# Kernel tuning notes

Measured on AMD Instinct MI355X. Metric: run time of the kernel, lower is better.

The kernel has to match this reference:

```python
import jax, jax.numpy as jnp
import numpy as np

N, K, A, LOCAL, PAIR = 1024, 48, 5, 512, 128
RBF_BINS = 16

def _normalize(v, eps=1e-8):
    return v / jnp.sqrt(jnp.sum(v * v, axis=-1, keepdims=True) + eps)

def _frames(pos):
    # pos: (N, A, 3); backbone frame from N(0), CA(1), C(2) via Gram-Schmidt
    n, ca, c = pos[:, 0], pos[:, 1], pos[:, 2]
    e1 = _normalize(c - ca)
    v2 = n - ca
    e2 = _normalize(v2 - jnp.sum(v2 * e1, -1, keepdims=True) * e1)
    e3 = jnp.cross(e1, e2)
    R = jnp.stack([e1, e2, e3], axis=-1)  # (N,3,3) columns are frame axes
    return R, ca

def _rbf(d, d_min=0.0, d_max=22.0, bins=RBF_BINS):
    centers = jnp.linspace(d_min, d_max, bins)
    step = (d_max - d_min) / bins
    return jnp.exp(-((d[..., None] - centers) / step) ** 2)

def setup_inputs():
    key = jax.random.key(0)
    ks = jax.random.split(key, 16)
    def rn(k, shape, scale=1.0):
        return (scale * jax.random.normal(k, shape)).astype(jnp.float32)
    local = rn(ks[0], (N, LOCAL))
    pos = rn(ks[1], (N, A, 3), 3.0)
    pair = rn(ks[2], (N, N, PAIR), 0.1)
    neighbours = jax.random.randint(ks[3], (N, K), 0, N).astype(jnp.int32)
    mask = jnp.ones((N,), dtype=bool)
    d_dist = A * A * RBF_BINS   # 400
    d_dir = A * A * 3           # 75
    d_vec = 2 * A * 3           # 30
    s = lambda f: 1.0 / np.sqrt(f)
    return dict(
        local=local, pos=pos, pair=pair, neighbours=neighbours, mask=mask,
        W_li=rn(ks[4], (LOCAL, PAIR), s(LOCAL)),
        W_lj=rn(ks[5], (LOCAL, PAIR), s(LOCAL)),
        W_dist=rn(ks[6], (d_dist, PAIR), s(d_dist)),
        W_dir=rn(ks[7], (d_dir, PAIR), s(d_dir)),
        W_rot=rn(ks[8], (9, PAIR), s(9)),
        W_vec=rn(ks[9], (d_vec, PAIR), s(d_vec)),
        ln_scale=jnp.ones((PAIR,), jnp.float32),
        ln_bias=jnp.zeros((PAIR,), jnp.float32),
        mlp_w1=rn(ks[10], (PAIR, 2 * PAIR), s(PAIR)),
        mlp_b1=jnp.zeros((2 * PAIR,), jnp.float32),
        mlp_w2=rn(ks[11], (2 * PAIR, PAIR), s(2 * PAIR)),
        mlp_b2=jnp.zeros((PAIR,), jnp.float32),
    )

def reference(local, pos, pair, neighbours, mask,
              W_li, W_lj, W_dist, W_dir, W_rot, W_vec,
              ln_scale, ln_bias, mlp_w1, mlp_b1, mlp_w2, mlp_b2):
    n_idx = jnp.arange(neighbours.shape[0])
    pair_mask = (mask[:, None] & mask[neighbours]) & (neighbours != -1)
    p = pair[n_idx[:, None], neighbours]                      # (N,K,PAIR) gather
    R, t = _frames(pos)                                       # (N,3,3), (N,3)
    pos_nb = pos[neighbours]                                  # (N,K,A,3)
    # source / target node feature projections
    p = p + (local @ W_li)[:, None] + (local @ W_lj)[neighbours]
    # distance features: all atom-pair distances, RBF-encoded in [0, 22]
    off = pos[:, None, :, None, :] - pos_nb[:, :, None, :, :] # (N,K,A,A,3)
    dist = jnp.sqrt(jnp.sum(off * off, -1) + 1e-8)            # (N,K,A,A)
    p = p + _rbf(dist).reshape(*neighbours.shape, -1) @ W_dist
    # direction features: atom-pair offsets in the local frame, normalized
    off_local = jnp.einsum('nij,nkabi->nkabj', R, off)
    p = p + _normalize(off_local).reshape(*neighbours.shape, -1) @ W_dir
    # relative rotation features: R_i^T R_j, flattened
    R_rel = jnp.einsum('nai,nkaj->nkij', R, R[neighbours])
    p = p + R_rel.reshape(*neighbours.shape, 9) @ W_rot
    # pair vector features: self and neighbour atoms in the local frame (x0.1)
    x_self = jnp.einsum('nij,nai->naj', R, pos - t[:, None])            # (N,A,3)
    x_nb = jnp.einsum('nij,nkai->nkaj', R, pos_nb - t[:, None, None])   # (N,K,A,3)
    vec = jnp.concatenate(
        (0.1 * jnp.broadcast_to(x_self[:, None], x_nb.shape), 0.1 * x_nb),
        axis=-1).reshape(*neighbours.shape, -1)
    p = p + vec @ W_vec
    # LayerNorm (scale + offset)
    mu = jnp.mean(p, -1, keepdims=True)
    var = jnp.var(p, -1, keepdims=True)
    p = (p - mu) * jax.lax.rsqrt(var + 1e-5) * ln_scale + ln_bias
    # MLP: hidden 2*PAIR, gelu, linear out
    p = jax.nn.gelu(p @ mlp_w1 + mlp_b1) @ mlp_w2 + mlp_b2
    return p, pair_mask
```

## Files before the change

### kernel.cpp

```cpp
#include <hip/hip_runtime.h>
#include <hip/hip_bf16.h>
#include <math.h>

#define N 1024
#define K 48
#define A 5
#define LOCALD 512
#define PAIRD 128
#define ROWS 32
#define FEATK 544
#define SF_STRIDE_B 1152

#define WS_R  0
#define WS_T  (WS_R + N*9)
#define WS_XS (WS_T + N*3)
#define WS_LI (WS_XS + N*15)
#define WS_LJ (WS_LI + N*128)
#define WCT_OFF 1159168u
#define W1T_OFF 1298432u
#define W2T_OFF 1363968u

typedef _Float16 half8 __attribute__((ext_vector_type(8)));
typedef float f32x16 __attribute__((ext_vector_type(16)));

__device__ __forceinline__ float gelu_fast(float x) {
    float u2 = 1.5957691216057308f * x * (1.0f + 0.044715f * x * x);
    float t = __expf(-u2);
    return x * __builtin_amdgcn_rcpf(1.0f + t);
}

__global__ __launch_bounds__(256) void prep_kernel(
    const float* __restrict__ local_, const float* __restrict__ pos,
    const float* __restrict__ W_li, const float* __restrict__ W_lj,
    const float* __restrict__ Wd, const float* __restrict__ Wdir,
    const float* __restrict__ Wrot, const float* __restrict__ Wv,
    const float* __restrict__ w1, const float* __restrict__ w2,
    float* __restrict__ ws, char* __restrict__ wsb)
{
    const int tid = threadIdx.x;
    if (blockIdx.x >= 256) {
        _Float16* wct = (_Float16*)(wsb + WCT_OFF);
        _Float16* w1t = (_Float16*)(wsb + W1T_OFF);
        _Float16* w2t = (_Float16*)(wsb + W2T_OFF);
        int g = (blockIdx.x - 256) * 256 + tid;
        if (g < 128 * 544) {
            int c = g & 127, f = g >> 7;
            float v = 0.0f;
            if (f < 400) v = Wd[(size_t)f * 128 + c];
            else if (f < 475) v = Wdir[(size_t)(f - 400) * 128 + c];
            else if (f < 484) v = Wrot[(size_t)(f - 475) * 128 + c];
            else if (f < 514) v = Wv[(size_t)(f - 484) * 128 + c];
            wct[(size_t)c * FEATK + f] = (_Float16)v;
        } else {
            int g2 = g - 128 * 544;
            if (g2 < 256 * 128) {
                int c = g2 & 255, f = g2 >> 8;
                w1t[(size_t)c * 128 + f] = (_Float16)w1[(size_t)f * 256 + c];
            } else {
                int g3 = g2 - 256 * 128;
                if (g3 < 128 * 256) {
                    int c = g3 & 127, f = g3 >> 7;
                    w2t[(size_t)c * 256 + f] = (_Float16)w2[(size_t)f * 128 + c];
                }
            }
        }
        return;
    }

    const int n0 = blockIdx.x * 4;
    __shared__ float sl[4][LOCALD];
    __shared__ float sR4[4][9];
    __shared__ float st4[4][3];

    for (int t = tid; t < 4 * LOCALD; t += 256) {
        int r = t >> 9, q = t & 511;
        sl[r][q] = local_[(size_t)(n0 + r) * LOCALD + q];
    }
    if (tid < 4) {
        int n = n0 + tid;
        const float* pp = pos + (size_t)n * 15;
        float nx = pp[0], ny = pp[1], nz = pp[2];
        float cax = pp[3], cay = pp[4], caz = pp[5];
        float cx = pp[6], cy = pp[7], cz = pp[8];
        float e1x = cx - cax, e1y = cy - cay, e1z = cz - caz;
        float inv1 = rsqrtf(e1x * e1x + e1y * e1y + e1z * e1z + 1e-8f);
        e1x *= inv1; e1y *= inv1; e1z *= inv1;
        float v2x = nx - cax, v2y = ny - cay, v2z = nz - caz;
        float dp = v2x * e1x + v2y * e1y + v2z * e1z;
        float e2x = v2x - dp * e1x, e2y = v2y - dp * e1y, e2z = v2z - dp * e1z;
        float inv2 = rsqrtf(e2x * e2x + e2y * e2y + e2z * e2z + 1e-8f);
        e2x *= inv2; e2y *= inv2; e2z *= inv2;
        float e3x = e1y * e2z - e1z * e2y;
        float e3y = e1z * e2x - e1x * e2z;
        float e3z = e1x * e2y - e1y * e2x;
        sR4[tid][0] = e1x; sR4[tid][1] = e2x; sR4[tid][2] = e3x;
        sR4[tid][3] = e1y; sR4[tid][4] = e2y; sR4[tid][5] = e3y;
        sR4[tid][6] = e1z; sR4[tid][7] = e2z; sR4[tid][8] = e3z;
        st4[tid][0] = cax; st4[tid][1] = cay; st4[tid][2] = caz;
        #pragma unroll
        for (int i = 0; i < 9; ++i) ws[WS_R + (size_t)n * 9 + i] = sR4[tid][i];
        #pragma unroll
        for (int i = 0; i < 3; ++i) ws[WS_T + (size_t)n * 3 + i] = st4[tid][i];
    }
    __syncthreads();

    for (int t = tid; t < 4 * 15; t += 256) {
        int r = t / 15, q = t % 15, a = q / 3, dd = q % 3;
        int n = n0 + r;
        const float* pp = pos + (size_t)n * 15 + a * 3;
        float v = sR4[r][0 * 3 + dd] * (pp[0] - st4[r][0])
                + sR4[r][1 * 3 + dd] * (pp[1] - st4[r][1])
                + sR4[r][2 * 3 + dd] * (pp[2] - st4[r][2]);
        ws[WS_XS + (size_t)n * 15 + q] = v;
    }

    const int c = tid & 127;
    const int hh = tid >> 7;
    const int r0 = hh * 2;
    float ali0 = 0, ali1 = 0, alj0 = 0, alj1 = 0;
    const float* wli = W_li + c;
    const float* wlj = W_lj + c;
    #pragma unroll 8
    for (int f = 0; f < LOCALD; ++f) {
        float a_ = wli[(size_t)f * 128];
        float b_ = wlj[(size_t)f * 128];
        float l0 = sl[r0 + 0][f], l1 = sl[r0 + 1][f];
        ali0 += l0 * a_; ali1 += l1 * a_;
        alj0 += l0 * b_; alj1 += l1 * b_;
    }
    ws[WS_LI + (size_t)(n0 + r0 + 0) * 128 + c] = ali0;
    ws[WS_LI + (size_t)(n0 + r0 + 1) * 128 + c] = ali1;
    ws[WS_LJ + (size_t)(n0 + r0 + 0) * 128 + c] = alj0;
    ws[WS_LJ + (size_t)(n0 + r0 + 1) * 128 + c] = alj1;
}

__device__ __forceinline__ void sfw(char* smem, int r, int f, float v) {
    int off = r * SF_STRIDE_B + ((f * 2) ^ ((r & 7) << 4));
    *(_Float16*)(smem + off) = (_Float16)v;
}

__global__ __launch_bounds__(256, 3) void main_kernel(
    const float* __restrict__ pair, const float* __restrict__ pos,
    const int* __restrict__ neigh, const int* __restrict__ mask,
    const float* __restrict__ ln_s, const float* __restrict__ ln_b,
    const float* __restrict__ b1, const float* __restrict__ b2,
    const float* __restrict__ ws, const char* __restrict__ wsb,
    float* __restrict__ out)
{
    const int R0 = blockIdx.x * ROWS;
    const int tid = threadIdx.x;
    const int lane = tid & 63;
    const int wv = tid >> 6;
    const int myrow = lane & 31;
    const int khalf = (lane >> 5) * 8;
    const int hi = lane >> 5;
    const int swz = (myrow & 7) << 4;

    __shared__ __align__(16) char smem[45184];
    int*   sn  = (int*)(smem + 36864);
    int*   sj  = (int*)(smem + 36992);
    float* spn = (float*)(smem + 37120);
    float* spj = (float*)(smem + 39040);
    float* srn = (float*)(smem + 40960);
    float* srj = (float*)(smem + 42112);
    float* sxs = (float*)(smem + 43264);

    const _Float16* wct = (const _Float16*)(wsb + WCT_OFF);
    const int colbase = wv * 32 + myrow;

    if (tid < ROWS) {
        int Rg = R0 + tid;
        int n = Rg / K;
        int kk = Rg - n * K;
        int j = neigh[n * K + kk];
        if (j < 0) j += N;
        sn[tid] = n; sj[tid] = j;
    }
    __syncthreads();

    const int n0 = R0 / K;
    const int n1 = (n0 + 1 < N) ? n0 + 1 : n0;
    float li0 = ws[WS_LI + (size_t)n0 * PAIRD + colbase];
    float li1 = ws[WS_LI + (size_t)n1 * PAIRD + colbase];
    float pv[16];
    #pragma unroll
    for (int q = 0; q < 16; ++q) {
        int rr = (q & 3) + 8 * (q >> 2) + 4 * hi;
        int nq = sn[rr], jq = sj[rr];
        float li = (nq == n0) ? li0 : li1;
        pv[q] = pair[((size_t)nq * N + jq) * PAIRD + colbase]
              + ws[WS_LJ + (size_t)jq * PAIRD + colbase] + li;
    }

    for (int t = tid; t < ROWS * 15; t += 256) {
        int r = t / 15, q = t % 15;
        spn[t] = pos[(size_t)sn[r] * 15 + q];
        spj[t] = pos[(size_t)sj[r] * 15 + q];
        sxs[t] = ws[WS_XS + (size_t)sn[r] * 15 + q];
    }
    for (int t = tid; t < ROWS * 9; t += 256) {
        int r = t / 9, q = t % 9;
        srn[t] = ws[WS_R + (size_t)sn[r] * 9 + q];
        srj[t] = ws[WS_R + (size_t)sj[r] * 9 + q];
    }
    __syncthreads();

    for (int t = tid; t < ROWS * 30; t += 256) {
        int r = t / 30, f = 514 + t % 30;
        sfw(smem, r, f, 0.0f);
    }

    for (int t = tid; t < ROWS * 25; t += 256) {
        int r = t / 25, ab = t % 25, a = ab / 5, b = ab % 5;
        const float* Pn = spn + r * 15;
        const float* Pj = spj + r * 15;
        const float* Rn = srn + r * 9;
        float o0 = Pn[a * 3 + 0] - Pj[b * 3 + 0];
        float o1 = Pn[a * 3 + 1] - Pj[b * 3 + 1];
        float o2 = Pn[a * 3 + 2] - Pj[b * 3 + 2];
        float d = sqrtf(o0 * o0 + o1 * o1 + o2 * o2 + 1e-8f);
        float z = d * (16.0f / 22.0f);
        int base = a * 80 + b * 16;
        int rb = r * SF_STRIDE_B;
        int rsw = (r & 7) << 4;
        #pragma unroll
        for (int bp = 0; bp < 8; ++bp) {
            float e0 = __expf(-z * z);
            float z1 = z - 1.0666666666666667f;
            float e1 = __expf(-z1 * z1);
            z = z1 - 1.0666666666666667f;
            union { _Float16 h[2]; unsigned u; } pk;
            pk.h[0] = (_Float16)e0; pk.h[1] = (_Float16)e1;
            int off = rb + (((base + bp * 2) * 2) ^ rsw);
            *(unsigned*)(smem + off) = pk.u;
        }
        float l0 = Rn[0] * o0 + Rn[3] * o1 + Rn[6] * o2;
        float l1 = Rn[1] * o0 + Rn[4] * o1 + Rn[7] * o2;
        float l2 = Rn[2] * o0 + Rn[5] * o1 + Rn[8] * o2;
        float inv = rsqrtf(l0 * l0 + l1 * l1 + l2 * l2 + 1e-8f);
        int dbase = 400 + a * 15 + b * 3;
        sfw(smem, r, dbase + 0, l0 * inv);
        sfw(smem, r, dbase + 1, l1 * inv);
        sfw(smem, r, dbase + 2, l2 * inv);
    }
    for (int t = tid; t < ROWS * 9; t += 256) {
        int r = t / 9, q = t % 9, i = q / 3, jd = q % 3;
        const float* Rn = srn + r * 9;
        const float* Rj = srj + r * 9;
        float v = Rn[0 * 3 + i] * Rj[0 * 3 + jd]
                + Rn[1 * 3 + i] * Rj[1 * 3 + jd]
                + Rn[2 * 3 + i] * Rj[2 * 3 + jd];
        sfw(smem, r, 475 + q, v);
    }
    for (int t = tid; t < ROWS * 15; t += 256) {
        int r = t / 15, q = t % 15, a = q / 3, dd = q % 3;
        const float* Pn = spn + r * 15;
        const float* Pj = spj + r * 15;
        const float* Rn = srn + r * 9;
        float xn = Rn[0 * 3 + dd] * (Pj[a * 3 + 0] - Pn[3])
                 + Rn[1 * 3 + dd] * (Pj[a * 3 + 1] - Pn[4])
                 + Rn[2 * 3 + dd] * (Pj[a * 3 + 2] - Pn[5]);
        sfw(smem, r, 484 + a * 6 + dd, 0.1f * sxs[r * 15 + q]);
        sfw(smem, r, 484 + a * 6 + 3 + dd, 0.1f * xn);
    }
    __syncthreads();

    f32x16 acc0, acc1;
    #pragma unroll
    for (int q = 0; q < 16; ++q) { acc0[q] = 0.0f; acc1[q] = 0.0f; }
    {
        const _Float16* wp = wct + (size_t)colbase * FEATK + khalf;
        #pragma unroll
        for (int ks = 0; ks < 34; ks += 2) {
            half8 b0 = *(const half8*)(wp + ks * 16);
            half8 b1 = *(const half8*)(wp + (ks + 1) * 16);
            int k0 = ks * 16 + khalf;
            int k1 = (ks + 1) * 16 + khalf;
            half8 a0 = *(const half8*)(smem + myrow * SF_STRIDE_B + ((k0 * 2) ^ swz));
            half8 a1 = *(const half8*)(smem + myrow * SF_STRIDE_B + ((k1 * 2) ^ swz));
            acc0 = __builtin_amdgcn_mfma_f32_32x32x16_f16(a0, b0, acc0, 0, 0, 0);
            acc1 = __builtin_amdgcn_mfma_f32_32x32x16_f16(a1, b1, acc1, 0, 0, 0);
        }
    }
    __syncthreads();

    #pragma unroll
    for (int q = 0; q < 16; ++q) {
        int rr = (q & 3) + 8 * (q >> 2) + 4 * hi;
        *(float*)(smem + rr * 512 + colbase * 4) = acc0[q] + acc1[q] + pv[q];
    }
    __syncthreads();

    {
        float lns0 = ln_s[lane], lns1 = ln_s[lane + 64];
        float lnb0 = ln_b[lane], lnb1 = ln_b[lane + 64];
        #pragma unroll
        for (int rr8 = 0; rr8 < 8; ++rr8) {
            int row = wv * 8 + rr8;
            float v0 = *(float*)(smem + row * 512 + lane * 4);
            float v1 = *(float*)(smem + row * 512 + (lane + 64) * 4);
            float s = v0 + v1, s2 = v0 * v0 + v1 * v1;
            #pragma unroll
            for (int o = 32; o > 0; o >>= 1) {
                s += __shfl_xor(s, o, 64);
                s2 += __shfl_xor(s2, o, 64);
            }
            float mu = s * (1.0f / 128.0f);
            float var = s2 * (1.0f / 128.0f) - mu * mu;
            float rs = rsqrtf(var + 1e-5f);
            int sw = (row & 7) << 4;
            *(_Float16*)(smem + 16384 + row * 256 + ((lane * 2) ^ sw)) =
                (_Float16)((v0 - mu) * rs * lns0 + lnb0);
            *(_Float16*)(smem + 16384 + row * 256 + (((lane + 64) * 2) ^ sw)) =
                (_Float16)((v1 - mu) * rs * lns1 + lnb1);
        }
    }
    __syncthreads();

    {
        const _Float16* w1t = (const _Float16*)(wsb + W1T_OFF);
        const int c0 = wv * 64 + myrow;
        const int c1 = c0 + 32;
        half8 wf0[8], wf1[8];
        #pragma unroll
        for (int ks = 0; ks < 8; ++ks) {
            wf0[ks] = *(const half8*)(w1t + (size_t)c0 * 128 + ks * 16 + khalf);
            wf1[ks] = *(const half8*)(w1t + (size_t)c1 * 128 + ks * 16 + khalf);
        }
        f32x16 h0, h1;
        #pragma unroll
        for (int q = 0; q < 16; ++q) { h0[q] = 0.0f; h1[q] = 0.0f; }
        #pragma unroll
        for (int ks = 0; ks < 8; ++ks) {
            int k0 = ks * 16 + khalf;
            half8 a = *(const half8*)(smem + 16384 + myrow * 256 + ((k0 * 2) ^ swz));
            h0 = __builtin_amdgcn_mfma_f32_32x32x16_f16(a, wf0[ks], h0, 0, 0, 0);
            h1 = __builtin_amdgcn_mfma_f32_32x32x16_f16(a, wf1[ks], h1, 0, 0, 0);
        }
        float bb0 = b1[c0], bb1 = b1[c1];
        #pragma unroll
        for (int q = 0; q < 16; ++q) {
            int rr = (q & 3) + 8 * (q >> 2) + 4 * hi;
            int sw = (rr & 7) << 4;
            *(_Float16*)(smem + rr * 512 + ((c0 * 2) ^ sw)) = (_Float16)gelu_fast(h0[q] + bb0);
            *(_Float16*)(smem + rr * 512 + ((c1 * 2) ^ sw)) = (_Float16)gelu_fast(h1[q] + bb1);
        }
    }
    __syncthreads();

    {
        const _Float16* w2t = (const _Float16*)(wsb + W2T_OFF);
        const int oc = wv * 32 + myrow;
        half8 w2f[16];
        #pragma unroll
        for (int ks = 0; ks < 16; ++ks)
            w2f[ks] = *(const half8*)(w2t + (size_t)oc * 256 + ks * 16 + khalf);
        f32x16 o0, o1;
        #pragma unroll
        for (int q = 0; q < 16; ++q) { o0[q] = 0.0f; o1[q] = 0.0f; }
        #pragma unroll
        for (int ks = 0; ks < 16; ks += 2) {
            int k0 = ks * 16 + khalf;
            int k1 = (ks + 1) * 16 + khalf;
            half8 a0 = *(const half8*)(smem + myrow * 512 + ((k0 * 2) ^ swz));
            half8 a1 = *(const half8*)(smem + myrow * 512 + ((k1 * 2) ^ swz));
            o0 = __builtin_amdgcn_mfma_f32_32x32x16_f16(a0, w2f[ks], o0, 0, 0, 0);
            o1 = __builtin_amdgcn_mfma_f32_32x32x16_f16(a1, w2f[ks + 1], o1, 0, 0, 0);
        }
        float bb = b2[oc];
        #pragma unroll
        for (int q = 0; q < 16; ++q) {
            int rr = (q & 3) + 8 * (q >> 2) + 4 * hi;
            out[((size_t)(R0 + rr)) * PAIRD + oc] = o0[q] + o1[q] + bb;
        }
    }

    if (tid < ROWS) {
        int Rg = R0 + tid;
        int n = Rg / K;
        int kk = Rg - n * K;
        int jr = neigh[n * K + kk];
        int jj = jr < 0 ? jr + N : jr;
        bool pm = (jr != -1) && (mask[n] != 0) && (mask[jj] != 0);
        out[(size_t)N * K * PAIRD + Rg] = pm ? 1.0f : 0.0f;
    }
}

extern "C" void kernel_launch(void* const* d_in, const int* in_sizes, int n_in,
                              void* d_out, int out_size, void* d_ws, size_t ws_size,
                              hipStream_t stream) {
    const float* local_ = (const float*)d_in[0];
    const float* pos = (const float*)d_in[1];
    const float* pair = (const float*)d_in[2];
    const int* neigh = (const int*)d_in[3];
    const int* mask = (const int*)d_in[4];
    const float* W_li = (const float*)d_in[5];
    const float* W_lj = (const float*)d_in[6];
    const float* W_dist = (const float*)d_in[7];
    const float* W_dir = (const float*)d_in[8];
    const float* W_rot = (const float*)d_in[9];
    const float* W_vec = (const float*)d_in[10];
    const float* ln_s = (const float*)d_in[11];
    const float* ln_b = (const float*)d_in[12];
    const float* w1 = (const float*)d_in[13];
    const float* b1 = (const float*)d_in[14];
    const float* w2 = (const float*)d_in[15];
    const float* b2 = (const float*)d_in[16];
    float* ws = (float*)d_ws;
    char* wsb = (char*)d_ws;
    float* out = (float*)d_out;

    hipLaunchKernelGGL(prep_kernel, dim3(256 + 528), dim3(256), 0, stream,
                       local_, pos, W_li, W_lj, W_dist, W_dir, W_rot, W_vec,
                       w1, w2, ws, wsb);
    hipLaunchKernelGGL(main_kernel, dim3((N * K) / ROWS), dim3(256), 0, stream,
                       pair, pos, neigh, mask, ln_s, ln_b, b1, b2, ws, wsb, out);
}
```

Baseline: 82.06 us.

## Recompute frames in main kernel, remap geometry features, raise occupancy

Drops the per-residue frame and self-coordinate precompute from the prep kernel. The main kernel now rebuilds rotation frames from the gathered positions in registers, which removes the workspace R/XS gathers and their shared buffers and cuts shared memory from about 45KB to 40KB. Geometry feature work is remapped so 8 threads handle each row. MLP weight fragments are loaded inside the MFMA loop instead of being preloaded, to lower register pressure, and launch bounds are raised to 4 blocks per SU. The cost is redundant frame math per row and less latency hiding on the weight loads.

```diff
diff --git a/kernel.cpp b/kernel.cpp
--- a/kernel.cpp
+++ b/kernel.cpp
@@ -11,10 +11,7 @@
 #define FEATK 544
 #define SF_STRIDE_B 1152
 
-#define WS_R  0
-#define WS_T  (WS_R + N*9)
-#define WS_XS (WS_T + N*3)
-#define WS_LI (WS_XS + N*15)
+#define WS_LI (N*9 + N*3 + N*15)
 #define WS_LJ (WS_LI + N*128)
 #define WCT_OFF 1159168u
 #define W1T_OFF 1298432u
@@ -29,8 +26,25 @@
     return x * __builtin_amdgcn_rcpf(1.0f + t);
 }
 
+__device__ __forceinline__ void frame_from(const float* __restrict__ P, float* __restrict__ R) {
+    float e1x = P[6] - P[3], e1y = P[7] - P[4], e1z = P[8] - P[5];
+    float inv1 = rsqrtf(e1x * e1x + e1y * e1y + e1z * e1z + 1e-8f);
+    e1x *= inv1; e1y *= inv1; e1z *= inv1;
+    float v2x = P[0] - P[3], v2y = P[1] - P[4], v2z = P[2] - P[5];
+    float dp = v2x * e1x + v2y * e1y + v2z * e1z;
+    float e2x = v2x - dp * e1x, e2y = v2y - dp * e1y, e2z = v2z - dp * e1z;
+    float inv2 = rsqrtf(e2x * e2x + e2y * e2y + e2z * e2z + 1e-8f);
+    e2x *= inv2; e2y *= inv2; e2z *= inv2;
+    float e3x = e1y * e2z - e1z * e2y;
+    float e3y = e1z * e2x - e1x * e2z;
+    float e3z = e1x * e2y - e1y * e2x;
+    R[0] = e1x; R[1] = e2x; R[2] = e3x;
+    R[3] = e1y; R[4] = e2y; R[5] = e3y;
+    R[6] = e1z; R[7] = e2z; R[8] = e3z;
+}
+
 __global__ __launch_bounds__(256) void prep_kernel(
-    const float* __restrict__ local_, const float* __restrict__ pos,
+    const float* __restrict__ local_,
     const float* __restrict__ W_li, const float* __restrict__ W_lj,
     const float* __restrict__ Wd, const float* __restrict__ Wdir,
     const float* __restrict__ Wrot, const float* __restrict__ Wv,
@@ -69,50 +83,11 @@
 
     const int n0 = blockIdx.x * 4;
     __shared__ float sl[4][LOCALD];
-    __shared__ float sR4[4][9];
-    __shared__ float st4[4][3];
-
     for (int t = tid; t < 4 * LOCALD; t += 256) {
         int r = t >> 9, q = t & 511;
         sl[r][q] = local_[(size_t)(n0 + r) * LOCALD + q];
     }
-    if (tid < 4) {
-        int n = n0 + tid;
-        const float* pp = pos + (size_t)n * 15;
-        float nx = pp[0], ny = pp[1], nz = pp[2];
-        float cax = pp[3], cay = pp[4], caz = pp[5];
-        float cx = pp[6], cy = pp[7], cz = pp[8];
-        float e1x = cx - cax, e1y = cy - cay, e1z = cz - caz;
-        float inv1 = rsqrtf(e1x * e1x + e1y * e1y + e1z * e1z + 1e-8f);
-        e1x *= inv1; e1y *= inv1; e1z *= inv1;
-        float v2x = nx - cax, v2y = ny - cay, v2z = nz - caz;
-        float dp = v2x * e1x + v2y * e1y + v2z * e1z;
-        float e2x = v2x - dp * e1x, e2y = v2y - dp * e1y, e2z = v2z - dp * e1z;
-        float inv2 = rsqrtf(e2x * e2x + e2y * e2y + e2z * e2z + 1e-8f);
-        e2x *= inv2; e2y *= inv2; e2z *= inv2;
-        float e3x = e1y * e2z - e1z * e2y;
-        float e3y = e1z * e2x - e1x * e2z;
-        float e3z = e1x * e2y - e1y * e2x;
-        sR4[tid][0] = e1x; sR4[tid][1] = e2x; sR4[tid][2] = e3x;
-        sR4[tid][3] = e1y; sR4[tid][4] = e2y; sR4[tid][5] = e3y;
-        sR4[tid][6] = e1z; sR4[tid][7] = e2z; sR4[tid][8] = e3z;
-        st4[tid][0] = cax; st4[tid][1] = cay; st4[tid][2] = caz;
-        #pragma unroll
-        for (int i = 0; i < 9; ++i) ws[WS_R + (size_t)n * 9 + i] = sR4[tid][i];
-        #pragma unroll
-        for (int i = 0; i < 3; ++i) ws[WS_T + (size_t)n * 3 + i] = st4[tid][i];
-    }
-    __syncthreads();
-
-    for (int t = tid; t < 4 * 15; t += 256) {
-        int r = t / 15, q = t % 15, a = q / 3, dd = q % 3;
-        int n = n0 + r;
-        const float* pp = pos + (size_t)n * 15 + a * 3;
-        float v = sR4[r][0 * 3 + dd] * (pp[0] - st4[r][0])
-                + sR4[r][1 * 3 + dd] * (pp[1] - st4[r][1])
-                + sR4[r][2 * 3 + dd] * (pp[2] - st4[r][2]);
-        ws[WS_XS + (size_t)n * 15 + q] = v;
-    }
+    __syncthreads();
 
     const int c = tid & 127;
     const int hh = tid >> 7;
@@ -139,7 +114,7 @@
     *(_Float16*)(smem + off) = (_Float16)v;
 }
 
-__global__ __launch_bounds__(256, 3) void main_kernel(
+__global__ __launch_bounds__(256, 4) void main_kernel(
     const float* __restrict__ pair, const float* __restrict__ pos,
     const int* __restrict__ neigh, const int* __restrict__ mask,
     const float* __restrict__ ln_s, const float* __restrict__ ln_b,
@@ -156,14 +131,11 @@
     const int hi = lane >> 5;
     const int swz = (myrow & 7) << 4;
 
-    __shared__ __align__(16) char smem[45184];
+    __shared__ __align__(16) char smem[40960];
     int*   sn  = (int*)(smem + 36864);
     int*   sj  = (int*)(smem + 36992);
     float* spn = (float*)(smem + 37120);
     float* spj = (float*)(smem + 39040);
-    float* srn = (float*)(smem + 40960);
-    float* srj = (float*)(smem + 42112);
-    float* sxs = (float*)(smem + 43264);
 
     const _Float16* wct = (const _Float16*)(wsb + WCT_OFF);
     const int colbase = wv * 32 + myrow;
@@ -178,16 +150,16 @@
     }
     __syncthreads();
 
-    const int n0 = R0 / K;
-    const int n1 = (n0 + 1 < N) ? n0 + 1 : n0;
-    float li0 = ws[WS_LI + (size_t)n0 * PAIRD + colbase];
-    float li1 = ws[WS_LI + (size_t)n1 * PAIRD + colbase];
+    const int nb0 = R0 / K;
+    const int nb1 = (nb0 + 1 < N) ? nb0 + 1 : nb0;
+    float li0 = ws[WS_LI + (size_t)nb0 * PAIRD + colbase];
+    float li1 = ws[WS_LI + (size_t)nb1 * PAIRD + colbase];
     float pv[16];
     #pragma unroll
     for (int q = 0; q < 16; ++q) {
         int rr = (q & 3) + 8 * (q >> 2) + 4 * hi;
         int nq = sn[rr], jq = sj[rr];
-        float li = (nq == n0) ? li0 : li1;
+        float li = (nq == nb0) ? li0 : li1;
         pv[q] = pair[((size_t)nq * N + jq) * PAIRD + colbase]
               + ws[WS_LJ + (size_t)jq * PAIRD + colbase] + li;
     }
@@ -196,72 +168,91 @@
         int r = t / 15, q = t % 15;
         spn[t] = pos[(size_t)sn[r] * 15 + q];
         spj[t] = pos[(size_t)sj[r] * 15 + q];
-        sxs[t] = ws[WS_XS + (size_t)sn[r] * 15 + q];
-    }
-    for (int t = tid; t < ROWS * 9; t += 256) {
-        int r = t / 9, q = t % 9;
-        srn[t] = ws[WS_R + (size_t)sn[r] * 9 + q];
-        srj[t] = ws[WS_R + (size_t)sj[r] * 9 + q];
-    }
-    __syncthreads();
-
-    for (int t = tid; t < ROWS * 30; t += 256) {
-        int r = t / 30, f = 514 + t % 30;
-        sfw(smem, r, f, 0.0f);
-    }
-
-    for (int t = tid; t < ROWS * 25; t += 256) {
-        int r = t / 25, ab = t % 25, a = ab / 5, b = ab % 5;
-        const float* Pn = spn + r * 15;
-        const float* Pj = spj + r * 15;
-        const float* Rn = srn + r * 9;
-        float o0 = Pn[a * 3 + 0] - Pj[b * 3 + 0];
-        float o1 = Pn[a * 3 + 1] - Pj[b * 3 + 1];
-        float o2 = Pn[a * 3 + 2] - Pj[b * 3 + 2];
-        float d = sqrtf(o0 * o0 + o1 * o1 + o2 * o2 + 1e-8f);
-        float z = d * (16.0f / 22.0f);
-        int base = a * 80 + b * 16;
-        int rb = r * SF_STRIDE_B;
-        int rsw = (r & 7) << 4;
-        #pragma unroll
-        for (int bp = 0; bp < 8; ++bp) {
-            float e0 = __expf(-z * z);
-            float z1 = z - 1.0666666666666667f;
-            float e1 = __expf(-z1 * z1);
-            z = z1 - 1.0666666666666667f;
-            union { _Float16 h[2]; unsigned u; } pk;
-            pk.h[0] = (_Float16)e0; pk.h[1] = (_Float16)e1;
-            int off = rb + (((base + bp * 2) * 2) ^ rsw);
-            *(unsigned*)(smem + off) = pk.u;
-        }
-        float l0 = Rn[0] * o0 + Rn[3] * o1 + Rn[6] * o2;
-        float l1 = Rn[1] * o0 + Rn[4] * o1 + Rn[7] * o2;
-        float l2 = Rn[2] * o0 + Rn[5] * o1 + Rn[8] * o2;
-        float inv = rsqrtf(l0 * l0 + l1 * l1 + l2 * l2 + 1e-8f);
-        int dbase = 400 + a * 15 + b * 3;
-        sfw(smem, r, dbase + 0, l0 * inv);
-        sfw(smem, r, dbase + 1, l1 * inv);
-        sfw(smem, r, dbase + 2, l2 * inv);
-    }
-    for (int t = tid; t < ROWS * 9; t += 256) {
-        int r = t / 9, q = t % 9, i = q / 3, jd = q % 3;
-        const float* Rn = srn + r * 9;
-        const float* Rj = srj + r * 9;
-        float v = Rn[0 * 3 + i] * Rj[0 * 3 + jd]
-                + Rn[1 * 3 + i] * Rj[1 * 3 + jd]
-                + Rn[2 * 3 + i] * Rj[2 * 3 + jd];
-        sfw(smem, r, 475 + q, v);
-    }
-    for (int t = tid; t < ROWS * 15; t += 256) {
-        int r = t / 15, q = t % 15, a = q / 3, dd = q % 3;
-        const float* Pn = spn + r * 15;
-        const float* Pj = spj + r * 15;
-        const float* Rn = srn + r * 9;
-        float xn = Rn[0 * 3 + dd] * (Pj[a * 3 + 0] - Pn[3])
-                 + Rn[1 * 3 + dd] * (Pj[a * 3 + 1] - Pn[4])
-                 + Rn[2 * 3 + dd] * (Pj[a * 3 + 2] - Pn[5]);
-        sfw(smem, r, 484 + a * 6 + dd, 0.1f * sxs[r * 15 + q]);
-        sfw(smem, r, 484 + a * 6 + 3 + dd, 0.1f * xn);
+    }
+    __syncthreads();
+
+    {
+        const int fr  = tid >> 3;
+        const int sub = tid & 7;
+        const float* Pn = spn + fr * 15;
+        const float* Pj = spj + fr * 15;
+
+        sfw(smem, fr, 514 + sub, 0.0f);
+        sfw(smem, fr, 522 + sub, 0.0f);
+        sfw(smem, fr, 530 + sub, 0.0f);
+        if (sub < 6) sfw(smem, fr, 538 + sub, 0.0f);
+
+        float rn[9];
+        frame_from(Pn, rn);
+
+        #pragma unroll
+        for (int m = 0; m < 4; ++m) {
+            int ab = sub + 8 * m;
+            if (ab < 25) {
+                int a = ab / 5, b = ab - 5 * (ab / 5);
+                float o0 = Pn[a * 3 + 0] - Pj[b * 3 + 0];
+                float o1 = Pn[a * 3 + 1] - Pj[b * 3 + 1];
+                float o2 = Pn[a * 3 + 2] - Pj[b * 3 + 2];
+                float d = sqrtf(o0 * o0 + o1 * o1 + o2 * o2 + 1e-8f);
+                float z = d * (16.0f / 22.0f);
+                int base = a * 80 + b * 16;
+                int rb = fr * SF_STRIDE_B;
+                int rsw = (fr & 7) << 4;
+                #pragma unroll
+                for (int bp = 0; bp < 8; ++bp) {
+                    float e0 = __expf(-z * z);
+                    float z1 = z - 1.0666666666666667f;
+                    float e1 = __expf(-z1 * z1);
+                    z = z1 - 1.0666666666666667f;
+                    union { _Float16 h[2]; unsigned u; } pk;
+                    pk.h[0] = (_Float16)e0; pk.h[1] = (_Float16)e1;
+                    int off = rb + (((base + bp * 2) * 2) ^ rsw);
+                    *(unsigned*)(smem + off) = pk.u;
+                }
+                float l0 = rn[0] * o0 + rn[3] * o1 + rn[6] * o2;
+                float l1 = rn[1] * o0 + rn[4] * o1 + rn[7] * o2;
+                float l2 = rn[2] * o0 + rn[5] * o1 + rn[8] * o2;
+                float inv = rsqrtf(l0 * l0 + l1 * l1 + l2 * l2 + 1e-8f);
+                int dbase = 400 + a * 15 + b * 3;
+                sfw(smem, fr, dbase + 0, l0 * inv);
+                sfw(smem, fr, dbase + 1, l1 * inv);
+                sfw(smem, fr, dbase + 2, l2 * inv);
+            }
+        }
+
+        #pragma unroll
+        for (int m = 0; m < 2; ++m) {
+            int task = (m == 0) ? sub : (sub < 2 ? 8 + sub : -1);
+            if (task >= 0) {
+                int a = task >> 1;
+                int kind = task & 1;
+                const float* Ps = kind ? Pj : Pn;
+                float v0 = Ps[a * 3 + 0] - Pn[3];
+                float v1 = Ps[a * 3 + 1] - Pn[4];
+                float v2 = Ps[a * 3 + 2] - Pn[5];
+                float x0 = rn[0] * v0 + rn[3] * v1 + rn[6] * v2;
+                float x1 = rn[1] * v0 + rn[4] * v1 + rn[7] * v2;
+                float x2 = rn[2] * v0 + rn[5] * v1 + rn[8] * v2;
+                int dbase = 484 + a * 6 + kind * 3;
+                sfw(smem, fr, dbase + 0, 0.1f * x0);
+                sfw(smem, fr, dbase + 1, 0.1f * x1);
+                sfw(smem, fr, dbase + 2, 0.1f * x2);
+            }
+        }
+
+        if (sub == 7) {
+            float rj[9];
+            frame_from(Pj, rj);
+            #pragma unroll
+            for (int i = 0; i < 3; ++i)
+                #pragma unroll
+                for (int jd = 0; jd < 3; ++jd) {
+                    float v = rn[0 * 3 + i] * rj[0 * 3 + jd]
+                            + rn[1 * 3 + i] * rj[1 * 3 + jd]
+                            + rn[2 * 3 + i] * rj[2 * 3 + jd];
+                    sfw(smem, fr, 475 + i * 3 + jd, v);
+                }
+        }
     }
     __syncthreads();
 
@@ -321,21 +312,19 @@
         const _Float16* w1t = (const _Float16*)(wsb + W1T_OFF);
         const int c0 = wv * 64 + myrow;
         const int c1 = c0 + 32;
-        half8 wf0[8], wf1[8];
+        const _Float16* wp0 = w1t + (size_t)c0 * 128 + khalf;
+        const _Float16* wp1 = w1t + (size_t)c1 * 128 + khalf;
+        f32x16 h0, h1;
+        #pragma unroll
+        for (int q = 0; q < 16; ++q) { h0[q] = 0.0f; h1[q] = 0.0f; }
         #pragma unroll
         for (int ks = 0; ks < 8; ++ks) {
-            wf0[ks] = *(const half8*)(w1t + (size_t)c0 * 128 + ks * 16 + khalf);
-            wf1[ks] = *(const half8*)(w1t + (size_t)c1 * 128 + ks * 16 + khalf);
-        }
-        f32x16 h0, h1;
-        #pragma unroll
-        for (int q = 0; q < 16; ++q) { h0[q] = 0.0f; h1[q] = 0.0f; }
-        #pragma unroll
-        for (int ks = 0; ks < 8; ++ks) {
+            half8 wf0 = *(const half8*)(wp0 + ks * 16);
+            half8 wf1 = *(const half8*)(wp1 + ks * 16);
             int k0 = ks * 16 + khalf;
             half8 a = *(const half8*)(smem + 16384 + myrow * 256 + ((k0 * 2) ^ swz));
-            h0 = __builtin_amdgcn_mfma_f32_32x32x16_f16(a, wf0[ks], h0, 0, 0, 0);
-            h1 = __builtin_amdgcn_mfma_f32_32x32x16_f16(a, wf1[ks], h1, 0, 0, 0);
+            h0 = __builtin_amdgcn_mfma_f32_32x32x16_f16(a, wf0, h0, 0, 0, 0);
+            h1 = __builtin_amdgcn_mfma_f32_32x32x16_f16(a, wf1, h1, 0, 0, 0);
         }
         float bb0 = b1[c0], bb1 = b1[c1];
         #pragma unroll
@@ -351,21 +340,20 @@
     {
         const _Float16* w2t = (const _Float16*)(wsb + W2T_OFF);
         const int oc = wv * 32 + myrow;
-        half8 w2f[16];
-        #pragma unroll
-        for (int ks = 0; ks < 16; ++ks)
-            w2f[ks] = *(const half8*)(w2t + (size_t)oc * 256 + ks * 16 + khalf);
+        const _Float16* wp = w2t + (size_t)oc * 256 + khalf;
         f32x16 o0, o1;
         #pragma unroll
         for (int q = 0; q < 16; ++q) { o0[q] = 0.0f; o1[q] = 0.0f; }
         #pragma unroll
         for (int ks = 0; ks < 16; ks += 2) {
+            half8 w0 = *(const half8*)(wp + ks * 16);
+            half8 w1f = *(const half8*)(wp + (ks + 1) * 16);
             int k0 = ks * 16 + khalf;
             int k1 = (ks + 1) * 16 + khalf;
             half8 a0 = *(const half8*)(smem + myrow * 512 + ((k0 * 2) ^ swz));
             half8 a1 = *(const half8*)(smem + myrow * 512 + ((k1 * 2) ^ swz));
-            o0 = __builtin_amdgcn_mfma_f32_32x32x16_f16(a0, w2f[ks], o0, 0, 0, 0);
-            o1 = __builtin_amdgcn_mfma_f32_32x32x16_f16(a1, w2f[ks + 1], o1, 0, 0, 0);
+            o0 = __builtin_amdgcn_mfma_f32_32x32x16_f16(a0, w0, o0, 0, 0, 0);
+            o1 = __builtin_amdgcn_mfma_f32_32x32x16_f16(a1, w1f, o1, 0, 0, 0);
         }
         float bb = b2[oc];
         #pragma unroll
@@ -411,7 +399,7 @@
     float* out = (float*)d_out;
 
     hipLaunchKernelGGL(prep_kernel, dim3(256 + 528), dim3(256), 0, stream,
-                       local_, pos, W_li, W_lj, W_dist, W_dir, W_rot, W_vec,
+                       local_, W_li, W_lj, W_dist, W_dir, W_rot, W_vec,
                        w1, w2, ws, wsb);
     hipLaunchKernelGGL(main_kernel, dim3((N * K) / ROWS), dim3(256), 0, stream,
                        pair, pos, neigh, mask, ln_s, ln_b, b1, b2, ws, wsb, out);
```

Result: slower. 83.75 us (+2.1%).
